# Kernel optimization log

Hardware: AMD Instinct MI355X
Metric: run time of the kernel (lower is better)

## Reference

```python
import jax, jax.numpy as jnp
import numpy as np

IN_CH = 512
EMB = 512

def setup_inputs() -> dict:
    key = jax.random.key(0)
    ks = jax.random.split(key, 14)
    s = 0.02
    inp = {
        'input': jax.random.normal(ks[0], (8, IN_CH, 64, 64), jnp.float32),
        'context': jax.random.normal(ks[1], (8, EMB, 32, 32), jnp.float32),
        # proj_in: Conv2d(in_channels, emb_dim, 1) -> weight [emb, in_ch]
        'proj_in_w': jax.random.normal(ks[2], (EMB, IN_CH), jnp.float32) * s,
        'proj_in_b': jnp.zeros((EMB,), jnp.float32),
        # Linear weights stored as [in, out] (math-equivalent to torch [out,in].T)
        'wq_w': jax.random.normal(ks[3], (EMB, EMB), jnp.float32) * s,
        'wq_b': jnp.zeros((EMB,), jnp.float32),
        'wk_w': jax.random.normal(ks[4], (EMB, EMB), jnp.float32) * s,
        'wk_b': jnp.zeros((EMB,), jnp.float32),
        'wv_w': jax.random.normal(ks[5], (EMB, EMB), jnp.float32) * s,
        'wv_b': jnp.zeros((EMB,), jnp.float32),
        # proj_out: Conv2d(emb+in_ch, in_ch, 1) -> weight [in_ch, emb+in_ch]
        'proj_out_w': jax.random.normal(ks[6], (IN_CH, EMB + IN_CH), jnp.float32) * s,
        'proj_out_b': jnp.zeros((IN_CH,), jnp.float32),
    }
    return inp

def reference(input, context, proj_in_w, proj_in_b, wq_w, wq_b, wk_w, wk_b,
              wv_w, wv_b, proj_out_w, proj_out_b):
    b, c_in, h, w = input.shape
    _, c_ctx, hc, wc = context.shape
    scale = EMB ** (-0.5)

    # context: [b, emb, hc, wc] -> [b, L, emb]
    ctx = context.reshape(b, c_ctx, hc * wc).transpose(0, 2, 1)

    # proj_in (1x1 conv) + flatten: [b, in_ch, h, w] -> [b, hw, emb]
    x = jnp.einsum('bchw,ec->bhwe', input, proj_in_w) + proj_in_b
    x = x.reshape(b, h * w, EMB)

    Q = x @ wq_w + wq_b                 # [b, hw, emb]
    K = ctx @ wk_w + wk_b               # [b, L, emb]
    V = ctx @ wv_w + wv_b               # [b, L, emb]

    att = jnp.einsum('bid,bjd->bij', Q, K) * scale  # [b, hw, L]
    att = jax.nn.softmax(att, axis=-1)
    out = jnp.einsum('bij,bjd->bid', att, V)        # [b, hw, emb]

    # [b, hw, emb] -> [b, emb, h, w]
    out = out.reshape(b, h, w, EMB).transpose(0, 3, 1, 2)
    out = jnp.concatenate([input, out], axis=1)     # [b, in_ch+emb, h, w]
    out = jnp.einsum('bchw,oc->bohw', out, proj_out_w) + proj_out_b[None, :, None, None]
    return out
```

## Files before the change

kernel.cpp:

```cpp
#include <hip/hip_runtime.h>
#include <hip/hip_bf16.h>

using bf16 = __hip_bfloat16;
typedef short s16x8 __attribute__((ext_vector_type(8)));
typedef float f32x4 __attribute__((ext_vector_type(4)));
typedef unsigned short u16;

__device__ __forceinline__ void gld_lds16(const void* g, void* l) {
  __builtin_amdgcn_global_load_lds(
      (const __attribute__((address_space(1))) void*)g,
      (__attribute__((address_space(3))) void*)l, 16, 0, 0);
}

__device__ __forceinline__ float bf2f(u16 u) {
  unsigned int x = ((unsigned int)u) << 16;
  return __builtin_bit_cast(float, x);
}

__global__ __launch_bounds__(256) void convert_f32_bf16(
    const float* __restrict__ in, bf16* __restrict__ out, int n) {
  int i = blockIdx.x * 256 + threadIdx.x;
  if (i < n) out[i] = __float2bfloat16(in[i]);
}

__global__ __launch_bounds__(256) void transpose_f32_to_bf16(
    const float* __restrict__ in, bf16* __restrict__ out, int inner,
    long in_b, long out_b, int out_ld, int coloff) {
  __shared__ float tile[32][33];
  const int bx = blockIdx.x;
  const int by = blockIdx.y;
  const int bz = blockIdx.z;
  const int tx = threadIdx.x & 31;
  const int ty = threadIdx.x >> 5;
  const float* ib = in + (long)bz * in_b;
  bf16* ob = out + (long)bz * out_b;
#pragma unroll
  for (int i = 0; i < 4; ++i) {
    int r = ty + i * 8;
    tile[r][tx] = ib[(long)(by * 32 + r) * inner + bx * 32 + tx];
  }
  __syncthreads();
#pragma unroll
  for (int i = 0; i < 4; ++i) {
    int r = ty + i * 8;
    ob[(long)(bx * 32 + r) * out_ld + coloff + by * 32 + tx] =
        __float2bfloat16(tile[tx][r]);
  }
}

__global__ __launch_bounds__(256) void bias_combine(
    const float* __restrict__ pb, const float* __restrict__ wq,
    const float* __restrict__ qb, float* __restrict__ out) {
  int o = blockIdx.x * 256 + threadIdx.x;
  if (o >= 512) return;
  float s = qb[o];
  for (int e = 0; e < 512; ++e) s += pb[e] * wq[e * 512 + o];
  out[o] = s;
}

__global__ __launch_bounds__(256) void rowinv_1024(
    const u16* __restrict__ S, float* __restrict__ inv) {
  const int t = threadIdx.x;
  const int w = t >> 6, lane = t & 63;
  const long row = (long)blockIdx.x * 4 + w;
  const u16* p = S + row * 1024 + lane * 16;
  s16x8 a = *(const s16x8*)p;
  s16x8 b = *(const s16x8*)(p + 8);
  float s = 0.f;
#pragma unroll
  for (int i = 0; i < 8; ++i) s += bf2f((u16)a[i]) + bf2f((u16)b[i]);
#pragma unroll
  for (int sh = 32; sh > 0; sh >>= 1) s += __shfl_xor(s, sh, 64);
  if (lane == 0) inv[row] = 1.0f / s;
}

template <int OUT_BF16, int BIAS_MODE, int EPI>
__global__ __launch_bounds__(256, 4) void gemm_bt_kernel(
    const bf16* __restrict__ A, long sAb, int lda,
    const bf16* __restrict__ B, long sBb, int ldb,
    void* __restrict__ Cp, long sCb, int ldc,
    const float* __restrict__ bias, const float* __restrict__ sc, long scb,
    float alpha, int K) {
  __shared__ __align__(16) bf16 tA[128 * 64];
  __shared__ __align__(16) bf16 tB[128 * 64];

  const int t = threadIdx.x;
  const int w = t >> 6;
  const int lane = t & 63;
  const int bn = blockIdx.x;
  const int bm = blockIdx.y;
  const int bz = blockIdx.z;

  const bf16* Ab = A + (long)bz * sAb;
  const bf16* Bb = B + (long)bz * sBb;

  const int srow = t >> 3;
  const int schunk = (t & 7) ^ (srow & 7);
  const int scol = schunk * 8;
  const long a_base = (long)(bm * 128 + srow) * lda + scol;
  const long b_base = (long)(bn * 128 + srow) * ldb + scol;
  char* lA = (char*)tA + w * 1024;
  char* lB = (char*)tB + w * 1024;

  const int wr = w >> 1, wc = w & 1;
  const int r15 = lane & 15;
  const int khalf = lane >> 4;
  f32x4 acc[4][4] = {};

  for (int kt = 0; kt < K; kt += 64) {
#pragma unroll
    for (int i = 0; i < 4; ++i) {
      gld_lds16(Ab + a_base + (long)(i * 32) * lda + kt, lA + i * 4096);
      gld_lds16(Bb + b_base + (long)(i * 32) * ldb + kt, lB + i * 4096);
    }
    __syncthreads();
#pragma unroll
    for (int kk = 0; kk < 2; ++kk) {
      const int chunk = kk * 4 + khalf;
      s16x8 af[4], bg[4];
#pragma unroll
      for (int m = 0; m < 4; ++m) {
        const int row = wr * 64 + m * 16 + r15;
        af[m] = *(const s16x8*)(tA + row * 64 + ((chunk ^ (row & 7)) * 8));
      }
#pragma unroll
      for (int n = 0; n < 4; ++n) {
        const int row = wc * 64 + n * 16 + r15;
        bg[n] = *(const s16x8*)(tB + row * 64 + ((chunk ^ (row & 7)) * 8));
      }
#pragma unroll
      for (int m = 0; m < 4; ++m)
#pragma unroll
        for (int n = 0; n < 4; ++n)
          acc[m][n] = __builtin_amdgcn_mfma_f32_16x16x32_bf16(af[m], bg[n],
                                                              acc[m][n], 0, 0, 0);
    }
    __syncthreads();
  }

#pragma unroll
  for (int m = 0; m < 4; ++m) {
    const int rb = bm * 128 + wr * 64 + m * 16 + (lane >> 4) * 4;
#pragma unroll
    for (int n = 0; n < 4; ++n) {
      const int col = bn * 128 + wc * 64 + n * 16 + (lane & 15);
      float bN = 0.f;
      if (BIAS_MODE == 1) bN = bias[col];
#pragma unroll
      for (int j = 0; j < 4; ++j) {
        const int row = rb + j;
        float v;
        if (EPI == 1) {
          v = __expf(acc[m][n][j] * alpha);
        } else if (EPI == 2) {
          v = acc[m][n][j] * sc[(long)bz * scb + row];
        } else {
          v = acc[m][n][j] * alpha;
          if (BIAS_MODE == 1) v += bN;
          if (BIAS_MODE == 2) v += bias[row];
        }
        const long off = (long)bz * sCb + (long)row * ldc + col;
        if (OUT_BF16)
          ((bf16*)Cp)[off] = __float2bfloat16(v);
        else
          ((float*)Cp)[off] = v;
      }
    }
  }
}

extern "C" void kernel_launch(void* const* d_in, const int* in_sizes, int n_in,
                              void* d_out, int out_size, void* d_ws, size_t ws_size,
                              hipStream_t stream) {
  const float* input   = (const float*)d_in[0];
  const float* context = (const float*)d_in[1];
  const float* pin_w   = (const float*)d_in[2];
  const float* pin_b   = (const float*)d_in[3];
  const float* wq_w    = (const float*)d_in[4];
  const float* wq_b    = (const float*)d_in[5];
  const float* wk_w    = (const float*)d_in[6];
  const float* wk_b    = (const float*)d_in[7];
  const float* wv_w    = (const float*)d_in[8];
  const float* wv_b    = (const float*)d_in[9];
  const float* pout_w  = (const float*)d_in[10];
  const float* pout_b  = (const float*)d_in[11];

  char* ws = (char*)d_ws;
  size_t off = 0;
  auto alloc = [&](size_t bytes) -> void* {
    void* p = ws + off;
    off += (bytes + 255) & ~(size_t)255;
    return p;
  };
  bf16* poutw = (bf16*)alloc((size_t)512 * 1024 * 2);
  bf16* wqT  = (bf16*)alloc((size_t)512 * 512 * 2);
  bf16* wkT  = (bf16*)alloc((size_t)512 * 512 * 2);
  bf16* wvT  = (bf16*)alloc((size_t)512 * 512 * 2);
  bf16* pinT = (bf16*)alloc((size_t)512 * 512 * 2);
  bf16* WQc  = (bf16*)alloc((size_t)512 * 512 * 2);
  float* bQc = (float*)alloc((size_t)512 * 4);
  bf16* cat  = (bf16*)alloc((size_t)32768 * 1024 * 2);
  bf16* ctxt = (bf16*)alloc((size_t)8192 * 512 * 2);
  bf16* Qb   = (bf16*)alloc((size_t)32768 * 512 * 2);
  bf16* Kmb  = (bf16*)alloc((size_t)8192 * 512 * 2);
  bf16* Vtb  = (bf16*)alloc((size_t)8 * 512 * 1024 * 2);
  bf16* Sb   = (bf16*)alloc((size_t)8 * 4096 * 1024 * 2);
  float* rinv = (float*)alloc((size_t)32768 * 4);

  dim3 blk(256);

  convert_f32_bf16<<<2048, blk, 0, stream>>>(pout_w, poutw, 512 * 1024);
  transpose_f32_to_bf16<<<dim3(16, 16, 1), blk, 0, stream>>>(wq_w, wqT, 512, 0, 0, 512, 0);
  transpose_f32_to_bf16<<<dim3(16, 16, 1), blk, 0, stream>>>(wk_w, wkT, 512, 0, 0, 512, 0);
  transpose_f32_to_bf16<<<dim3(16, 16, 1), blk, 0, stream>>>(wv_w, wvT, 512, 0, 0, 512, 0);
  transpose_f32_to_bf16<<<dim3(16, 16, 1), blk, 0, stream>>>(pin_w, pinT, 512, 0, 0, 512, 0);
  bias_combine<<<2, blk, 0, stream>>>(pin_b, wq_w, wq_b, bQc);
  transpose_f32_to_bf16<<<dim3(128, 16, 8), blk, 0, stream>>>(
      input, cat, 4096, (long)512 * 4096, (long)4096 * 1024, 1024, 0);
  transpose_f32_to_bf16<<<dim3(32, 16, 8), blk, 0, stream>>>(
      context, ctxt, 1024, (long)512 * 1024, (long)1024 * 512, 512, 0);

  const float scale = 0.04419417382415922f;

  gemm_bt_kernel<1, 0, 0><<<dim3(4, 4, 1), blk, 0, stream>>>(
      wqT, 0, 512, pinT, 0, 512, WQc, 0, 512, nullptr, nullptr, 0, 1.f, 512);
  gemm_bt_kernel<1, 1, 0><<<dim3(4, 256, 1), blk, 0, stream>>>(
      cat, 0, 1024, WQc, 0, 512, Qb, 0, 512, bQc, nullptr, 0, 1.f, 512);
  gemm_bt_kernel<1, 1, 0><<<dim3(4, 64, 1), blk, 0, stream>>>(
      ctxt, 0, 512, wkT, 0, 512, Kmb, 0, 512, wk_b, nullptr, 0, 1.f, 512);
  gemm_bt_kernel<1, 2, 0><<<dim3(8, 4, 8), blk, 0, stream>>>(
      wvT, 0, 512, ctxt, (long)1024 * 512, 512, Vtb, (long)512 * 1024, 1024,
      wv_b, nullptr, 0, 1.f, 512);
  gemm_bt_kernel<1, 0, 1><<<dim3(8, 32, 8), blk, 0, stream>>>(
      Qb, (long)4096 * 512, 512, Kmb, (long)1024 * 512, 512, Sb,
      (long)4096 * 1024, 1024, nullptr, nullptr, 0, scale, 512);
  rowinv_1024<<<dim3(8192, 1, 1), blk, 0, stream>>>((const u16*)Sb, rinv);
  gemm_bt_kernel<1, 0, 2><<<dim3(4, 32, 8), blk, 0, stream>>>(
      Sb, (long)4096 * 1024, 1024, Vtb, (long)512 * 1024, 1024,
      (void*)(cat + 512), (long)4096 * 1024, 1024, nullptr, rinv, 4096, 1.f, 1024);
  gemm_bt_kernel<0, 2, 0><<<dim3(32, 4, 8), blk, 0, stream>>>(
      poutw, 0, 1024, cat, (long)4096 * 1024, 1024, d_out,
      (long)512 * 4096, 4096, pout_b, nullptr, 0, 1.f, 1024);
}
```

Baseline: 404.2 us.

## Fuse softmax row sums into QK epilogue and remap workgroups per XCD

The QK^T GEMM epilogue now accumulates the exp row sums with shuffles and atomics into a zeroed buffer, which removes the separate rowinv pass that re-read the full score matrix. The PV GEMM takes the reciprocal once per row instead of loading the scale per element. All GEMMs switch to a 1D grid whose block index is remapped so that consecutive tiles land on the same XCD, aiming for better L2 reuse. The cost is contention from the atomics, an extra zeroing kernel, and summing in fp32 before the bf16 rounding of S, which slightly changes numerics.

```diff
diff --git a/kernel.cpp b/kernel.cpp
--- a/kernel.cpp
+++ b/kernel.cpp
@@ -21,6 +21,11 @@
     const float* __restrict__ in, bf16* __restrict__ out, int n) {
   int i = blockIdx.x * 256 + threadIdx.x;
   if (i < n) out[i] = __float2bfloat16(in[i]);
+}
+
+__global__ __launch_bounds__(256) void zero_f32(float* __restrict__ p, int n) {
+  int i = blockIdx.x * 256 + threadIdx.x;
+  if (i < n) p[i] = 0.f;
 }
 
 __global__ __launch_bounds__(256) void transpose_f32_to_bf16(
@@ -58,38 +63,29 @@
   out[o] = s;
 }
 
-__global__ __launch_bounds__(256) void rowinv_1024(
-    const u16* __restrict__ S, float* __restrict__ inv) {
-  const int t = threadIdx.x;
-  const int w = t >> 6, lane = t & 63;
-  const long row = (long)blockIdx.x * 4 + w;
-  const u16* p = S + row * 1024 + lane * 16;
-  s16x8 a = *(const s16x8*)p;
-  s16x8 b = *(const s16x8*)(p + 8);
-  float s = 0.f;
-#pragma unroll
-  for (int i = 0; i < 8; ++i) s += bf2f((u16)a[i]) + bf2f((u16)b[i]);
-#pragma unroll
-  for (int sh = 32; sh > 0; sh >>= 1) s += __shfl_xor(s, sh, 64);
-  if (lane == 0) inv[row] = 1.0f / s;
-}
-
 template <int OUT_BF16, int BIAS_MODE, int EPI>
 __global__ __launch_bounds__(256, 4) void gemm_bt_kernel(
     const bf16* __restrict__ A, long sAb, int lda,
     const bf16* __restrict__ B, long sBb, int ldb,
     void* __restrict__ Cp, long sCb, int ldc,
-    const float* __restrict__ bias, const float* __restrict__ sc, long scb,
-    float alpha, int K) {
+    const float* __restrict__ bias, float* __restrict__ sc, long scb,
+    float alpha, int K, int lgx, int lgy) {
   __shared__ __align__(16) bf16 tA[128 * 64];
   __shared__ __align__(16) bf16 tB[128 * 64];
+
+  const int nwg = gridDim.x;
+  const int orig = blockIdx.x;
+  const int q = nwg >> 3, r = nwg & 7;
+  const int xcd = orig & 7, local = orig >> 3;
+  const int wgid = (xcd < r ? xcd * (q + 1) : r * (q + 1) + (xcd - r) * q) + local;
+  const int bn = wgid & ((1 << lgx) - 1);
+  const int tmp = wgid >> lgx;
+  const int bm = tmp & ((1 << lgy) - 1);
+  const int bz = tmp >> lgy;
 
   const int t = threadIdx.x;
   const int w = t >> 6;
   const int lane = t & 63;
-  const int bn = blockIdx.x;
-  const int bm = blockIdx.y;
-  const int bz = blockIdx.z;
 
   const bf16* Ab = A + (long)bz * sAb;
   const bf16* Bb = B + (long)bz * sBb;
@@ -141,9 +137,15 @@
 #pragma unroll
   for (int m = 0; m < 4; ++m) {
     const int rb = bm * 128 + wr * 64 + m * 16 + (lane >> 4) * 4;
+    float rin[4];
+    if (EPI == 2) {
+#pragma unroll
+      for (int j = 0; j < 4; ++j) rin[j] = 1.0f / sc[(long)bz * scb + rb + j];
+    }
+    float rs[4] = {0.f, 0.f, 0.f, 0.f};
 #pragma unroll
     for (int n = 0; n < 4; ++n) {
-      const int col = bn * 128 + wc * 64 + n * 16 + (lane & 15);
+      const int col = bn * 128 + wc * 64 + n * 16 + r15;
       float bN = 0.f;
       if (BIAS_MODE == 1) bN = bias[col];
 #pragma unroll
@@ -152,8 +154,9 @@
         float v;
         if (EPI == 1) {
           v = __expf(acc[m][n][j] * alpha);
+          rs[j] += v;
         } else if (EPI == 2) {
-          v = acc[m][n][j] * sc[(long)bz * scb + row];
+          v = acc[m][n][j] * rin[j];
         } else {
           v = acc[m][n][j] * alpha;
           if (BIAS_MODE == 1) v += bN;
@@ -164,6 +167,15 @@
           ((bf16*)Cp)[off] = __float2bfloat16(v);
         else
           ((float*)Cp)[off] = v;
+      }
+    }
+    if (EPI == 1) {
+#pragma unroll
+      for (int j = 0; j < 4; ++j) {
+        float s = rs[j];
+#pragma unroll
+        for (int sh = 1; sh < 16; sh <<= 1) s += __shfl_xor(s, sh, 64);
+        if (r15 == 0) atomicAdd(sc + (long)bz * scb + rb + j, s);
       }
     }
   }
@@ -205,11 +217,12 @@
   bf16* Kmb  = (bf16*)alloc((size_t)8192 * 512 * 2);
   bf16* Vtb  = (bf16*)alloc((size_t)8 * 512 * 1024 * 2);
   bf16* Sb   = (bf16*)alloc((size_t)8 * 4096 * 1024 * 2);
-  float* rinv = (float*)alloc((size_t)32768 * 4);
+  float* rsum = (float*)alloc((size_t)32768 * 4);
 
   dim3 blk(256);
 
   convert_f32_bf16<<<2048, blk, 0, stream>>>(pout_w, poutw, 512 * 1024);
+  zero_f32<<<128, blk, 0, stream>>>(rsum, 32768);
   transpose_f32_to_bf16<<<dim3(16, 16, 1), blk, 0, stream>>>(wq_w, wqT, 512, 0, 0, 512, 0);
   transpose_f32_to_bf16<<<dim3(16, 16, 1), blk, 0, stream>>>(wk_w, wkT, 512, 0, 0, 512, 0);
   transpose_f32_to_bf16<<<dim3(16, 16, 1), blk, 0, stream>>>(wv_w, wvT, 512, 0, 0, 512, 0);
@@ -222,23 +235,23 @@
 
   const float scale = 0.04419417382415922f;
 
-  gemm_bt_kernel<1, 0, 0><<<dim3(4, 4, 1), blk, 0, stream>>>(
-      wqT, 0, 512, pinT, 0, 512, WQc, 0, 512, nullptr, nullptr, 0, 1.f, 512);
-  gemm_bt_kernel<1, 1, 0><<<dim3(4, 256, 1), blk, 0, stream>>>(
-      cat, 0, 1024, WQc, 0, 512, Qb, 0, 512, bQc, nullptr, 0, 1.f, 512);
-  gemm_bt_kernel<1, 1, 0><<<dim3(4, 64, 1), blk, 0, stream>>>(
-      ctxt, 0, 512, wkT, 0, 512, Kmb, 0, 512, wk_b, nullptr, 0, 1.f, 512);
-  gemm_bt_kernel<1, 2, 0><<<dim3(8, 4, 8), blk, 0, stream>>>(
+  gemm_bt_kernel<1, 0, 0><<<dim3(16), blk, 0, stream>>>(
+      wqT, 0, 512, pinT, 0, 512, WQc, 0, 512, nullptr, nullptr, 0, 1.f, 512, 2, 2);
+  gemm_bt_kernel<1, 1, 0><<<dim3(1024), blk, 0, stream>>>(
+      cat, 0, 1024, WQc, 0, 512, Qb, 0, 512, bQc, nullptr, 0, 1.f, 512, 2, 8);
+  gemm_bt_kernel<1, 1, 0><<<dim3(256), blk, 0, stream>>>(
+      ctxt, 0, 512, wkT, 0, 512, Kmb, 0, 512, wk_b, nullptr, 0, 1.f, 512, 2, 6);
+  gemm_bt_kernel<1, 2, 0><<<dim3(256), blk, 0, stream>>>(
       wvT, 0, 512, ctxt, (long)1024 * 512, 512, Vtb, (long)512 * 1024, 1024,
-      wv_b, nullptr, 0, 1.f, 512);
-  gemm_bt_kernel<1, 0, 1><<<dim3(8, 32, 8), blk, 0, stream>>>(
+      wv_b, nullptr, 0, 1.f, 512, 3, 2);
+  gemm_bt_kernel<1, 0, 1><<<dim3(2048), blk, 0, stream>>>(
       Qb, (long)4096 * 512, 512, Kmb, (long)1024 * 512, 512, Sb,
-      (long)4096 * 1024, 1024, nullptr, nullptr, 0, scale, 512);
-  rowinv_1024<<<dim3(8192, 1, 1), blk, 0, stream>>>((const u16*)Sb, rinv);
-  gemm_bt_kernel<1, 0, 2><<<dim3(4, 32, 8), blk, 0, stream>>>(
+      (long)4096 * 1024, 1024, nullptr, rsum, 4096, scale, 512, 3, 5);
+  gemm_bt_kernel<1, 0, 2><<<dim3(1024), blk, 0, stream>>>(
       Sb, (long)4096 * 1024, 1024, Vtb, (long)512 * 1024, 1024,
-      (void*)(cat + 512), (long)4096 * 1024, 1024, nullptr, rinv, 4096, 1.f, 1024);
-  gemm_bt_kernel<0, 2, 0><<<dim3(32, 4, 8), blk, 0, stream>>>(
+      (void*)(cat + 512), (long)4096 * 1024, 1024, nullptr, rsum, 4096, 1.f,
+      1024, 2, 5);
+  gemm_bt_kernel<0, 2, 0><<<dim3(1024), blk, 0, stream>>>(
       poutw, 0, 1024, cat, (long)4096 * 1024, 1024, d_out,
-      (long)512 * 4096, 4096, pout_b, nullptr, 0, 1.f, 1024);
-}
+      (long)512 * 4096, 4096, pout_b, nullptr, 0, 1.f, 1024, 5, 2);
+}
```

Measured after the change: 380.6 us. 1.06x faster.
